# Optimization experiments

Hardware: AMD Instinct MI355X
Metric: run time of the kernel (lower is better)

Reference implementation:

```python
import jax, jax.numpy as jnp
import numpy as np

B, N, DIN, DH = 16, 512, 128, 256
NEG = -9.0e15  # matches -9000000000000000.0 in torch source


def _xavier(key, fan_in, fan_out):
    lim = float(np.sqrt(6.0 / (fan_in + fan_out)))
    return jax.random.uniform(key, (fan_in, fan_out), jnp.float32, -lim, lim)


def _l2n(x, eps=1e-12):
    # torch F.normalize: x / max(||x||, eps)
    return x / jnp.maximum(jnp.linalg.norm(x, axis=-1, keepdims=True), eps)


def _prelu(x, a):
    return jnp.where(x >= 0, x, a * x)


def setup_inputs() -> dict:
    key = jax.random.key(0)
    ks = jax.random.split(key, 12)
    seq = jax.random.normal(ks[0], (B, N, DIN), jnp.float32)
    # sparse-ish nonnegative adjacency with self loops, row-normalized
    u = jax.random.uniform(ks[1], (B, N, N), jnp.float32)
    a = jnp.where(u < 0.1, u, 0.0) + jnp.eye(N, dtype=jnp.float32)[None]
    adj = a / a.sum(-1, keepdims=True)
    # dense diffusion matrix, row-normalized
    d = jax.random.uniform(ks[2], (B, N, N), jnp.float32)
    diff = d / d.sum(-1, keepdims=True)
    # dropout keep-mask for F.dropout(p=0.1, training=True)
    keep = jax.random.bernoulli(ks[3], 0.9, (B, N, N)).astype(jnp.float32)
    drop_mask = keep / 0.9
    return {
        "seq": seq, "adj": adj, "diff": diff, "drop_mask": drop_mask,
        "fc1_w": _xavier(ks[4], DIN, DH),
        "q_w": _xavier(ks[5], DH, DH),
        "k_w": _xavier(ks[6], DH, DH),
        "v_w1": _xavier(ks[7], DH, DH),
        "v_w2": _xavier(ks[8], DH, DH),
        "fc2_w": _xavier(ks[9], DIN, DH),
        "bias1": jnp.zeros((DH,), jnp.float32),
        "bias2": jnp.zeros((DH,), jnp.float32),
        "prelu1_a": jnp.float32(0.25),
        "prelu2_a": jnp.float32(0.25),
        "v_prelu_a": jnp.float32(0.25),
    }


def reference(seq, adj, diff, drop_mask, fc1_w, q_w, k_w, v_w1, v_w2,
              fc2_w, bias1, bias2, prelu1_a, prelu2_a, v_prelu_a):
    # ---- GCN1 (attention branch) ----
    fts = seq @ fc1_w                                   # [B,N,H]
    out = jnp.einsum('bmn,bnh->bmh', adj, fts)          # adj aggregation
    q = _l2n(out @ q_w)
    k = _l2n(out @ k_w)
    scores = jax.lax.stop_gradient(jnp.einsum('bmd,bnd->bmn', q, k))  # .detach()
    div_loss = jnp.mean(jnp.sum((q - k) ** 2, axis=-1))
    att = jnp.where(adj > 0, scores, NEG)
    att = jax.nn.softmax(att, axis=-1) * drop_mask      # dropout(p=0.1)
    agg = jnp.einsum('bmn,bnh->bmh', att, out)
    v = _prelu(agg @ v_w1, v_prelu_a) @ v_w2 + bias1
    h1 = _prelu(v, prelu1_a)
    # ---- GCN2 (plain branch) ----
    h2 = _prelu(jnp.einsum('bmn,bnh->bmh', diff, seq @ fc2_w) + bias2, prelu2_a)
    # ---- Readout ----
    c1 = jnp.mean(h1, axis=1)                           # [B,H]
    c2 = jnp.mean(h2, axis=1)
    # ---- DIS ----
    n1 = _l2n(h1).reshape(B * N, DH)
    n2 = _l2n(h2).reshape(B * N, DH)
    node_logits = n1 @ n2.T                             # [B*N, B*N]
    graph_logits = _l2n(c1) @ _l2n(c2).T                # [B, B]
    return node_logits, graph_logits, div_loss
```

## Files before the change

### kernel.cpp

```cpp
#include <hip/hip_runtime.h>
#include <hip/hip_bf16.h>


using bf16x8 = __attribute__((ext_vector_type(8))) short;
using f32x4  = __attribute__((ext_vector_type(4))) float;

__device__ __forceinline__ unsigned short f2b(float f) {
    union { float f; unsigned int u; } x; x.f = f;
    unsigned int r = x.u + 0x7FFFu + ((x.u >> 16) & 1u);
    return (unsigned short)(r >> 16);
}
__device__ __forceinline__ void gload_lds16(const void* g, void* l) {
    __builtin_amdgcn_global_load_lds(
        (const __attribute__((address_space(1))) void*)g,
        (__attribute__((address_space(3))) void*)l, 16, 0, 0);
}
__device__ __forceinline__ bf16x8 ldfrag(const unsigned short* p) {
    return *reinterpret_cast<const bf16x8*>(p);
}

__global__ __launch_bounds__(256) void prep(
    const float* __restrict__ seq, const float* __restrict__ adj,
    const float* __restrict__ diff,
    const float* __restrict__ fc1, const float* __restrict__ fc2,
    const float* __restrict__ qw,  const float* __restrict__ kw,
    const float* __restrict__ v1,  const float* __restrict__ v2,
    unsigned short* __restrict__ seq_bf, unsigned short* __restrict__ adj_bf,
    unsigned short* __restrict__ diff_bf,
    unsigned short* fc1T, unsigned short* fc2T, unsigned short* qwT,
    unsigned short* kwT,  unsigned short* v1T,  unsigned short* v2T)
{
    __shared__ float t[32][33];
    const int bid = blockIdx.x, tid = threadIdx.x;
    if (bid < 9216) {
        long i = (long)bid * 256 + tid;
        const float* src; unsigned short* dst; long off;
        if (i < 262144)       { src = seq;  dst = seq_bf;  off = i; }
        else if (i < 1310720) { src = adj;  dst = adj_bf;  off = i - 262144; }
        else                  { src = diff; dst = diff_bf; off = i - 1310720; }
        float4 v = reinterpret_cast<const float4*>(src)[off];
        ushort4 o; o.x = f2b(v.x); o.y = f2b(v.y); o.z = f2b(v.z); o.w = f2b(v.w);
        reinterpret_cast<ushort4*>(dst)[off] = o;
        return;
    }
    const int r = bid - 9216;
    const int z = r >> 6;
    const float* in; unsigned short* op; int R;
    if      (z == 0) { in = fc1; op = fc1T; R = 128; }
    else if (z == 1) { in = fc2; op = fc2T; R = 128; }
    else if (z == 2) { in = qw;  op = qwT;  R = 256; }
    else if (z == 3) { in = kw;  op = kwT;  R = 256; }
    else if (z == 4) { in = v1;  op = v1T;  R = 256; }
    else             { in = v2;  op = v2T;  R = 256; }
    const int c0 = (r & 7) * 32, r0 = ((r >> 3) & 7) * 32;
    if (r0 >= R) return;
    const int x = tid & 31, y = tid >> 5;
    for (int i = 0; i < 32; i += 8) t[y + i][x] = in[(long)(r0 + y + i) * 256 + c0 + x];
    __syncthreads();
    for (int i = 0; i < 32; i += 8)
        op[(long)(c0 + y + i) * R + r0 + x] = f2b(t[x][y + i]);
}

#define BN 128
#define BK 64

template<int TBM, bool WF, bool WB, bool SWZ, bool RD>
__global__ __launch_bounds__(256) void gemm_nt(
    const unsigned short* __restrict__ A, const unsigned short* __restrict__ Bt,
    float* __restrict__ Cf, unsigned short* __restrict__ Cb,
    int M, int Nn, int K, int lda, int ldb, int ldc,
    long sA, long sB, long sC,
    const float* __restrict__ rd_psum1, const float* __restrict__ rd_psum2,
    const float* __restrict__ rd_rowpart,
    float* __restrict__ rd_outg, float* __restrict__ rd_outdiv)
{
    constexpr int MI = TBM / 32;
    __shared__ unsigned char smem_g[(TBM + BN) * BK * 2];
    __shared__ float rd_invn[32];
    __shared__ float rd_red[4];
    unsigned short* As = (unsigned short*)smem_g;
    unsigned short* Bs = (unsigned short*)(smem_g + TBM * BK * 2);
    const int b = blockIdx.z;
    A  += (long)b * sA;
    Bt += (long)b * sB;
    const long cbase = (long)b * sC;

    int tx, ty;
    if (SWZ) {
        int bid = blockIdx.y * gridDim.x + blockIdx.x;
        int nwg = gridDim.x * gridDim.y;
        int cpx = nwg >> 3;
        int s = (bid & 7) * cpx + (bid >> 3);
        tx = s % gridDim.x; ty = s / gridDim.x;
    } else { tx = blockIdx.x; ty = blockIdx.y; }
    const int tile_m = ty * TBM;
    const int tile_n = tx * BN;

    const int tid  = threadIdx.x;
    const int lane = tid & 63;
    const int wave = tid >> 6;
    const int wm = (wave >> 1) * (TBM / 2);
    const int wn = (wave & 1) << 6;
    const int lrow = lane >> 3;
    const int lcol = (lane & 7) << 3;

    f32x4 acc[MI][4] = {};

    for (int k0 = 0; k0 < K; k0 += BK) {
        #pragma unroll
        for (int i = 0; i < TBM / 32; ++i) {
            const int rb = (i * 4 + wave) * 8;
            gload_lds16(A + (long)(tile_m + rb + lrow) * lda + k0 + lcol, &As[rb * BK]);
        }
        #pragma unroll
        for (int i = 0; i < 4; ++i) {
            const int rb = (i * 4 + wave) * 8;
            gload_lds16(Bt + (long)(tile_n + rb + lrow) * ldb + k0 + lcol, &Bs[rb * BK]);
        }
        __syncthreads();
        #pragma unroll
        for (int ks = 0; ks < 2; ++ks) {
            const int kk = ks * 32 + ((lane >> 4) << 3);
            bf16x8 af[MI], bq[4];
            #pragma unroll
            for (int mi = 0; mi < MI; ++mi)
                af[mi] = ldfrag(&As[(wm + (lane & 15) + mi * 16) * BK + kk]);
            #pragma unroll
            for (int ni = 0; ni < 4; ++ni)
                bq[ni] = ldfrag(&Bs[(wn + (lane & 15) + ni * 16) * BK + kk]);
            #pragma unroll
            for (int mi = 0; mi < MI; ++mi)
                #pragma unroll
                for (int ni = 0; ni < 4; ++ni)
                    acc[mi][ni] = __builtin_amdgcn_mfma_f32_16x16x32_bf16(
                        af[mi], bq[ni], acc[mi][ni], 0, 0, 0);
        }
        __syncthreads();
    }

    const int c0 = lane & 15;
    const int r0 = (lane >> 4) << 2;

    if (WB) {
        #pragma unroll
        for (int ni = 0; ni < 4; ++ni) {
            const int col = tile_n + wn + ni * 16 + c0;
            #pragma unroll
            for (int mi = 0; mi < MI; ++mi) {
                const int row0 = tile_m + wm + mi * 16 + r0;
                #pragma unroll
                for (int j = 0; j < 4; ++j)
                    Cb[cbase + (long)(row0 + j) * ldc + col] = f2b(acc[mi][ni][j]);
            }
        }
    }
    if (WF) {
        float* bounce = (float*)smem_g;
        const int tr = tid >> 5;
        const int tc = (tid & 31) << 2;
        #pragma unroll
        for (int h = 0; h < 2; ++h) {
            __syncthreads();
            if ((wave >> 1) == h) {
                #pragma unroll
                for (int mi = 0; mi < MI; ++mi)
                    #pragma unroll
                    for (int ni = 0; ni < 4; ++ni)
                        #pragma unroll
                        for (int j = 0; j < 4; ++j)
                            bounce[(mi * 16 + r0 + j) * 128 + wn + ni * 16 + c0] =
                                acc[mi][ni][j];
            }
            __syncthreads();
            #pragma unroll
            for (int p = 0; p < 8; ++p) {
                const int rl = p * 8 + tr;
                f32x4 v = *reinterpret_cast<const f32x4*>(&bounce[rl * 128 + tc]);
                __builtin_nontemporal_store(v, reinterpret_cast<f32x4*>(
                    &Cf[cbase + (long)(tile_m + h * 64 + rl) * ldc + tile_n + tc]));
            }
        }
    }
    if (RD) {
        if (blockIdx.x == 0 && blockIdx.y == 0) {
            __syncthreads();
            float* c1s = (float*)smem_g;
            float* c2s = c1s + 4096;
            const int t = tid;
            for (int g = 0; g < 16; ++g) {
                float s1 = 0.f, s2 = 0.f;
                #pragma unroll
                for (int c = 0; c < 16; ++c) {
                    s1 += rd_psum1[(long)(g * 16 + c) * 256 + t];
                    s2 += rd_psum2[(long)(g * 16 + c) * 256 + t];
                }
                c1s[g * 256 + t] = s1 * (1.f / 512.f);
                c2s[g * 256 + t] = s2 * (1.f / 512.f);
            }
            __syncthreads();
            if (t < 32) {
                const float* row = (t < 16) ? &c1s[t * 256] : &c2s[(t - 16) * 256];
                float ss = 0.f;
                for (int h = 0; h < 256; ++h) { float v = row[h]; ss += v * v; }
                rd_invn[t] = 1.f / fmaxf(sqrtf(ss), 1e-12f);
            }
            __syncthreads();
            const int ii = t >> 4, jj = t & 15;
            float s = 0.f;
            for (int h = 0; h < 256; ++h) s += c1s[ii * 256 + h] * c2s[jj * 256 + h];
            rd_outg[ii * 16 + jj] = s * rd_invn[ii] * rd_invn[16 + jj];
            float ds = 0.f;
            for (int i = t; i < 8192; i += 256) ds += rd_rowpart[i];
            #pragma unroll
            for (int o = 32; o; o >>= 1) ds += __shfl_xor(ds, o);
            if ((t & 63) == 0) rd_red[t >> 6] = ds;
            __syncthreads();
            if (t == 0)
                rd_outdiv[0] = (rd_red[0] + rd_red[1] + rd_red[2] + rd_red[3]) * (1.f / 8192.f);
        }
    }
}

__global__ __launch_bounds__(256) void gcn1qk(
    const unsigned short* __restrict__ adj_bf,
    const unsigned short* __restrict__ ftsT,
    const unsigned short* __restrict__ qkT,
    unsigned short* __restrict__ outT,
    unsigned short* __restrict__ q_bf,
    unsigned short* __restrict__ k_bf)
{
    __shared__ unsigned short Ot[16 * 264];
    __shared__ float sred[16][4];

    const int b  = blockIdx.y;
    const int m0 = blockIdx.x << 4;
    const int tid = threadIdx.x, lane = tid & 63, wave = tid >> 6;
    const int hi = lane >> 4, c0 = lane & 15, r0 = hi << 2;
    const int ko = hi << 3;

    {
        const int wn = wave << 6;
        const unsigned short* ap = adj_bf + ((long)b * 512 + m0 + c0) * 512;
        f32x4 acc[4] = {};
        #pragma unroll 2
        for (int k0 = 0; k0 < 512; k0 += 32) {
            bf16x8 af = ldfrag(ap + k0 + ko);
            #pragma unroll
            for (int ni = 0; ni < 4; ++ni) {
                bf16x8 bq = ldfrag(ftsT + (long)(wn + ni * 16 + c0) * 8192 + b * 512 + k0 + ko);
                acc[ni] = __builtin_amdgcn_mfma_f32_16x16x32_bf16(af, bq, acc[ni], 0, 0, 0);
            }
        }
        #pragma unroll
        for (int ni = 0; ni < 4; ++ni) {
            const int col = wn + ni * 16 + c0;
            ushort4 o;
            unsigned short* e = (unsigned short*)&o;
            #pragma unroll
            for (int j = 0; j < 4; ++j) {
                unsigned short v = f2b(acc[ni][j]);
                e[j] = v;
                Ot[(r0 + j) * 264 + col] = v;
            }
            *reinterpret_cast<ushort4*>(
                &outT[(long)b * 131072 + (long)col * 512 + m0 + r0]) = o;
        }
    }
    __syncthreads();

    {
        const int wn = wave << 7;
        f32x4 acc[8] = {};
        #pragma unroll 2
        for (int k0 = 0; k0 < 256; k0 += 32) {
            bf16x8 af = ldfrag(&Ot[c0 * 264 + k0 + ko]);
            #pragma unroll
            for (int ni = 0; ni < 8; ++ni) {
                bf16x8 bq = ldfrag(qkT + (long)(wn + ni * 16 + c0) * 256 + k0 + ko);
                acc[ni] = __builtin_amdgcn_mfma_f32_16x16x32_bf16(af, bq, acc[ni], 0, 0, 0);
            }
        }
        float rs[4] = {};
        #pragma unroll
        for (int ni = 0; ni < 8; ++ni)
            #pragma unroll
            for (int j = 0; j < 4; ++j) { float x = acc[ni][j]; rs[j] += x * x; }
        #pragma unroll
        for (int o = 1; o <= 8; o <<= 1)
            #pragma unroll
            for (int j = 0; j < 4; ++j) rs[j] += __shfl_xor(rs[j], o);
        if (c0 == 0) {
            #pragma unroll
            for (int j = 0; j < 4; ++j) sred[r0 + j][wave] = rs[j];
        }
        __syncthreads();
        float inv[4];
        #pragma unroll
        for (int j = 0; j < 4; ++j) {
            const int rr = r0 + j;
            float sq = sred[rr][0] + sred[rr][1];
            float sk = sred[rr][2] + sred[rr][3];
            inv[j] = 1.f / fmaxf(sqrtf(wave < 2 ? sq : sk), 1e-12f);
        }
        #pragma unroll
        for (int ni = 0; ni < 8; ++ni)
            #pragma unroll
            for (int j = 0; j < 4; ++j) {
                const long rowg = (long)b * 512 + m0 + r0 + j;
                const int col = wn + ni * 16 + c0;
                unsigned short v = f2b(acc[ni][j] * inv[j]);
                if (wave < 2) q_bf[rowg * 256 + col] = v;
                else          k_bf[rowg * 256 + col - 256] = v;
            }
    }
}

__global__ __launch_bounds__(256) void attmlp_h2(
    const unsigned short* __restrict__ q_bf,
    const unsigned short* __restrict__ k_bf,
    const unsigned short* __restrict__ adj_bf,
    const float* __restrict__ drop,
    const unsigned short* __restrict__ outT,
    const unsigned short* __restrict__ w1T,
    const unsigned short* __restrict__ w2T,
    const float* __restrict__ bias1,
    const float* __restrict__ av, const float* __restrict__ a1,
    unsigned short* __restrict__ n1,
    float* __restrict__ psum1,
    float* __restrict__ rowpart,
    const unsigned short* __restrict__ diff_bf,
    const unsigned short* __restrict__ fts2T,
    const float* __restrict__ bias2, const float* __restrict__ a2,
    unsigned short* __restrict__ n2,
    float* __restrict__ psum2)
{
    __shared__ unsigned char smem[33280];
    __shared__ float redm[32][4], reds[32][4];

    const int idx = blockIdx.x >> 1;
    const int tid = threadIdx.x, lane = tid & 63, wave = tid >> 6;
    const int hi = lane >> 4, c0 = lane & 15, r0 = hi << 2;
    const int ko = hi << 3;

    if (blockIdx.x & 1) {
        unsigned short* Pls = (unsigned short*)smem;
        unsigned short* T   = (unsigned short*)smem;

        const int b  = idx >> 4;
        const int m0 = (idx & 15) << 5;
        const unsigned short* qp = q_bf + (long)b * 131072;
        const unsigned short* kp = k_bf + (long)b * 131072;
        const unsigned short* ot = outT + (long)b * 131072;
        const unsigned short* ap = adj_bf + ((long)b * 512 + m0) * 512;
        const float*          dp = drop   + ((long)b * 512 + m0) * 512;

        {
            const int wn = wave << 7;
            f32x4 acc[2][8] = {};
            #pragma unroll 2
            for (int k0 = 0; k0 < 256; k0 += 32) {
                bf16x8 af[2];
                #pragma unroll
                for (int mi = 0; mi < 2; ++mi)
                    af[mi] = ldfrag(qp + (long)(m0 + mi * 16 + c0) * 256 + k0 + ko);
                #pragma unroll
                for (int ni = 0; ni < 8; ++ni) {
                    bf16x8 bq = ldfrag(kp + (long)(wn + ni * 16 + c0) * 256 + k0 + ko);
                    #pragma unroll
                    for (int mi = 0; mi < 2; ++mi)
                        acc[mi][ni] = __builtin_amdgcn_mfma_f32_16x16x32_bf16(
                            af[mi], bq, acc[mi][ni], 0, 0, 0);
                }
            }

            float rmax[2][4];
            #pragma unroll
            for (int mi = 0; mi < 2; ++mi)
                #pragma unroll
                for (int j = 0; j < 4; ++j) rmax[mi][j] = -3.0e38f;
            #pragma unroll
            for (int mi = 0; mi < 2; ++mi)
                #pragma unroll
                for (int ni = 0; ni < 8; ++ni)
                    #pragma unroll
                    for (int j = 0; j < 4; ++j) {
                        const int rowl = mi * 16 + r0 + j;
                        const int col  = wn + ni * 16 + c0;
                        float s = acc[mi][ni][j];
                        if (col == m0 + rowl)
                            rowpart[(long)b * 512 + m0 + rowl] = 2.f - 2.f * s;
                        bool m = ap[(long)rowl * 512 + col] != 0;
                        s = m ? s : -3.0e38f;
                        acc[mi][ni][j] = s;
                        rmax[mi][j] = fmaxf(rmax[mi][j], s);
                    }
            #pragma unroll
            for (int o = 1; o <= 8; o <<= 1)
                #pragma unroll
                for (int mi = 0; mi < 2; ++mi)
                    #pragma unroll
                    for (int j = 0; j < 4; ++j)
                        rmax[mi][j] = fmaxf(rmax[mi][j], __shfl_xor(rmax[mi][j], o));
            if (c0 == 0) {
                #pragma unroll
                for (int mi = 0; mi < 2; ++mi)
                    #pragma unroll
                    for (int j = 0; j < 4; ++j) redm[mi * 16 + r0 + j][wave] = rmax[mi][j];
            }
            __syncthreads();
            float mx[2][4], rsum[2][4];
            #pragma unroll
            for (int mi = 0; mi < 2; ++mi)
                #pragma unroll
                for (int j = 0; j < 4; ++j) {
                    const int rr = mi * 16 + r0 + j;
                    mx[mi][j] = fmaxf(fmaxf(redm[rr][0], redm[rr][1]),
                                      fmaxf(redm[rr][2], redm[rr][3]));
                    rsum[mi][j] = 0.f;
                }
            #pragma unroll
            for (int mi = 0; mi < 2; ++mi)
                #pragma unroll
                for (int ni = 0; ni < 8; ++ni)
                    #pragma unroll
                    for (int j = 0; j < 4; ++j) {
                        float e = __expf(acc[mi][ni][j] - mx[mi][j]);
                        acc[mi][ni][j] = e;
                        rsum[mi][j] += e;
                    }
            #pragma unroll
            for (int o = 1; o <= 8; o <<= 1)
                #pragma unroll
                for (int mi = 0; mi < 2; ++mi)
                    #pragma unroll
                    for (int j = 0; j < 4; ++j) rsum[mi][j] += __shfl_xor(rsum[mi][j], o);
            if (c0 == 0) {
                #pragma unroll
                for (int mi = 0; mi < 2; ++mi)
                    #pragma unroll
                    for (int j = 0; j < 4; ++j) reds[mi * 16 + r0 + j][wave] = rsum[mi][j];
            }
            __syncthreads();
            float inv[2][4];
            #pragma unroll
            for (int mi = 0; mi < 2; ++mi)
                #pragma unroll
                for (int j = 0; j < 4; ++j) {
                    const int rr = mi * 16 + r0 + j;
                    inv[mi][j] = 1.f / (reds[rr][0] + reds[rr][1] + reds[rr][2] + reds[rr][3]);
                }
            #pragma unroll
            for (int mi = 0; mi < 2; ++mi)
                #pragma unroll
                for (int ni = 0; ni < 8; ++ni)
                    #pragma unroll
                    for (int j = 0; j < 4; ++j) {
                        const int rowl = mi * 16 + r0 + j;
                        const int col  = wn + ni * 16 + c0;
                        float p = acc[mi][ni][j] * inv[mi][j] * dp[(long)rowl * 512 + col];
                        Pls[rowl * 520 + col] = f2b(p);
                    }
        }
        __syncthreads();

        f32x4 acc2[2][4] = {};
        {
            const int wn = wave << 6;
            #pragma unroll 2
            for (int k0 = 0; k0 < 512; k0 += 32) {
                bf16x8 af[2];
                #pragma unroll
                for (int mi = 0; mi < 2; ++mi)
                    af[mi] = ldfrag(&Pls[(mi * 16 + c0) * 520 + k0 + ko]);
                #pragma unroll
                for (int ni = 0; ni < 4; ++ni) {
                    bf16x8 bq = ldfrag(ot + (long)(wn + ni * 16 + c0) * 512 + k0 + ko);
                    #pragma unroll
                    for (int mi = 0; mi < 2; ++mi)
                        acc2[mi][ni] = __builtin_amdgcn_mfma_f32_16x16x32_bf16(
                            af[mi], bq, acc2[mi][ni], 0, 0, 0);
                }
            }
        }
        __syncthreads();

        const int wn6 = wave << 6;
        const float alphav = av[0];
        #pragma unroll
        for (int mi = 0; mi < 2; ++mi)
            #pragma unroll
            for (int ni = 0; ni < 4; ++ni)
                #pragma unroll
                for (int j = 0; j < 4; ++j)
                    T[(mi * 16 + r0 + j) * 264 + wn6 + ni * 16 + c0] = f2b(acc2[mi][ni][j]);
        __syncthreads();
        f32x4 acct[2][4] = {};
        #pragma unroll 2
        for (int k0 = 0; k0 < 256; k0 += 32) {
            bf16x8 af[2];
            #pragma unroll
            for (int mi = 0; mi < 2; ++mi)
                af[mi] = ldfrag(&T[(mi * 16 + c0) * 264 + k0 + ko]);
            #pragma unroll
            for (int ni = 0; ni < 4; ++ni) {
                bf16x8 bq = ldfrag(w1T + (long)(wn6 + ni * 16 + c0) * 256 + k0 + ko);
                #pragma unroll
                for (int mi = 0; mi < 2; ++mi)
                    acct[mi][ni] = __builtin_amdgcn_mfma_f32_16x16x32_bf16(
                        af[mi], bq, acct[mi][ni], 0, 0, 0);
            }
        }
        __syncthreads();
        #pragma unroll
        for (int mi = 0; mi < 2; ++mi)
            #pragma unroll
            for (int ni = 0; ni < 4; ++ni)
                #pragma unroll
                for (int j = 0; j < 4; ++j) {
                    float x = acct[mi][ni][j];
                    x = (x >= 0.f) ? x : alphav * x;
                    T[(mi * 16 + r0 + j) * 264 + wn6 + ni * 16 + c0] = f2b(x);
                }
        __syncthreads();

        f32x4 acc3[2][4] = {};
        #pragma unroll 2
        for (int k0 = 0; k0 < 256; k0 += 32) {
            bf16x8 af[2];
            #pragma unroll
            for (int mi = 0; mi < 2; ++mi)
                af[mi] = ldfrag(&T[(mi * 16 + c0) * 264 + k0 + ko]);
            #pragma unroll
            for (int ni = 0; ni < 4; ++ni) {
                bf16x8 bq = ldfrag(w2T + (long)(wn6 + ni * 16 + c0) * 256 + k0 + ko);
                #pragma unroll
                for (int mi = 0; mi < 2; ++mi)
                    acc3[mi][ni] = __builtin_amdgcn_mfma_f32_16x16x32_bf16(
                        af[mi], bq, acc3[mi][ni], 0, 0, 0);
            }
        }

        const float alpha1 = a1[0];
        float rs[2][4] = {};
        #pragma unroll
        for (int ni = 0; ni < 4; ++ni) {
            const float bv = bias1[wn6 + ni * 16 + c0];
            #pragma unroll
            for (int mi = 0; mi < 2; ++mi)
                #pragma unroll
                for (int j = 0; j < 4; ++j) {
                    float x = acc3[mi][ni][j] + bv;
                    x = (x >= 0.f) ? x : alpha1 * x;
                    acc3[mi][ni][j] = x;
                    rs[mi][j] += x * x;
                }
        }
        #pragma unroll
        for (int o = 1; o <= 8; o <<= 1)
            #pragma unroll
            for (int mi = 0; mi < 2; ++mi)
                #pragma unroll
                for (int j = 0; j < 4; ++j) rs[mi][j] += __shfl_xor(rs[mi][j], o);
        __syncthreads();
        if (c0 == 0) {
            #pragma unroll
            for (int mi = 0; mi < 2; ++mi)
                #pragma unroll
                for (int j = 0; j < 4; ++j) redm[mi * 16 + r0 + j][wave] = rs[mi][j];
        }
        __syncthreads();
        float inv2[2][4];
        #pragma unroll
        for (int mi = 0; mi < 2; ++mi)
            #pragma unroll
            for (int j = 0; j < 4; ++j) {
                const int rr = mi * 16 + r0 + j;
                float s = redm[rr][0] + redm[rr][1] + redm[rr][2] + redm[rr][3];
                inv2[mi][j] = 1.f / fmaxf(sqrtf(s), 1e-12f);
            }
        float cs[4];
        #pragma unroll
        for (int ni = 0; ni < 4; ++ni) {
            float s = 0.f;
            #pragma unroll
            for (int mi = 0; mi < 2; ++mi)
                #pragma unroll
                for (int j = 0; j < 4; ++j) s += acc3[mi][ni][j];
            s += __shfl_xor(s, 16);
            s += __shfl_xor(s, 32);
            cs[ni] = s;
        }
        if (lane < 16) {
            #pragma unroll
            for (int ni = 0; ni < 4; ++ni)
                psum1[(long)idx * 256 + wn6 + ni * 16 + lane] = cs[ni];
        }
        const long row0g = (long)b * 512 + m0;
        #pragma unroll
        for (int mi = 0; mi < 2; ++mi)
            #pragma unroll
            for (int ni = 0; ni < 4; ++ni)
                #pragma unroll
                for (int j = 0; j < 4; ++j)
                    n1[(row0g + mi * 16 + r0 + j) * 256 + wn6 + ni * 16 + c0] =
                        f2b(acc3[mi][ni][j] * inv2[mi][j]);
    } else {
        const int z = idx >> 4;
        const int arow0 = (idx & 15) << 5;
        const unsigned short* ad = diff_bf + (long)z * 262144;
        const unsigned short* bt = fts2T + z * 512;
        const int wn = wave << 6;

        f32x4 acc[2][4] = {};
        #pragma unroll 2
        for (int k0 = 0; k0 < 512; k0 += 32) {
            bf16x8 af[2];
            #pragma unroll
            for (int mi = 0; mi < 2; ++mi)
                af[mi] = ldfrag(ad + (long)(arow0 + mi * 16 + c0) * 512 + k0 + ko);
            #pragma unroll
            for (int ni = 0; ni < 4; ++ni) {
                bf16x8 bq = ldfrag(bt + (long)(wn + ni * 16 + c0) * 8192 + k0 + ko);
                #pragma unroll
                for (int mi = 0; mi < 2; ++mi)
                    acc[mi][ni] = __builtin_amdgcn_mfma_f32_16x16x32_bf16(
                        af[mi], bq, acc[mi][ni], 0, 0, 0);
            }
        }

        const float alpha = a2[0];
        float rs[2][4] = {};
        #pragma unroll
        for (int ni = 0; ni < 4; ++ni) {
            const float bv = bias2[wn + ni * 16 + c0];
            #pragma unroll
            for (int mi = 0; mi < 2; ++mi)
                #pragma unroll
                for (int j = 0; j < 4; ++j) {
                    float x = acc[mi][ni][j] + bv;
                    x = (x >= 0.f) ? x : alpha * x;
                    acc[mi][ni][j] = x;
                    rs[mi][j] += x * x;
                }
        }
        #pragma unroll
        for (int o = 1; o <= 8; o <<= 1)
            #pragma unroll
            for (int mi = 0; mi < 2; ++mi)
                #pragma unroll
                for (int j = 0; j < 4; ++j) rs[mi][j] += __shfl_xor(rs[mi][j], o);
        if (c0 == 0) {
            #pragma unroll
            for (int mi = 0; mi < 2; ++mi)
                #pragma unroll
                for (int j = 0; j < 4; ++j) redm[mi * 16 + r0 + j][wave] = rs[mi][j];
        }
        __syncthreads();
        float inv[2][4];
        #pragma unroll
        for (int mi = 0; mi < 2; ++mi)
            #pragma unroll
            for (int j = 0; j < 4; ++j) {
                const int rr = mi * 16 + r0 + j;
                float s = redm[rr][0] + redm[rr][1] + redm[rr][2] + redm[rr][3];
                inv[mi][j] = 1.f / fmaxf(sqrtf(s), 1e-12f);
            }
        float cs[4];
        #pragma unroll
        for (int ni = 0; ni < 4; ++ni) {
            float s = 0.f;
            #pragma unroll
            for (int mi = 0; mi < 2; ++mi)
                #pragma unroll
                for (int j = 0; j < 4; ++j) s += acc[mi][ni][j];
            s += __shfl_xor(s, 16);
            s += __shfl_xor(s, 32);
            cs[ni] = s;
        }
        if (lane < 16) {
            #pragma unroll
            for (int ni = 0; ni < 4; ++ni)
                psum2[(long)idx * 256 + wn + ni * 16 + lane] = cs[ni];
        }
        const long grow0 = (long)idx * 32;
        #pragma unroll
        for (int mi = 0; mi < 2; ++mi)
            #pragma unroll
            for (int ni = 0; ni < 4; ++ni)
                #pragma unroll
                for (int j = 0; j < 4; ++j)
                    n2[(grow0 + mi * 16 + r0 + j) * 256 + wn + ni * 16 + c0] =
                        f2b(acc[mi][ni][j] * inv[mi][j]);
    }
}

static constexpr long OFF_SEQ_BF  = 0;
static constexpr long OFF_FC1T    = 2097152;
static constexpr long OFF_QWT     = 2228224;
static constexpr long OFF_VW1T    = 2490368;
static constexpr long OFF_VW2T    = 2621440;
static constexpr long OFF_ADJ     = 3145728;
static constexpr long OFF_DIFF    = 11534336;
static constexpr long OFF_FTST    = 19922944;
static constexpr long OFF_OUTT    = 28311552;
static constexpr long OFF_QBF     = 32505856;
static constexpr long OFF_KBF     = 36700160;
static constexpr long OFF_N1      = 40894464;
static constexpr long OFF_N2      = 45088768;
static constexpr long OFF_PSUM    = 49283072;
static constexpr long OFF_ROWPART = 49807360;

extern "C" void kernel_launch(void* const* d_in, const int* in_sizes, int n_in,
                              void* d_out, int out_size, void* d_ws, size_t ws_size,
                              hipStream_t stream) {
    const float* seq      = (const float*)d_in[0];
    const float* adj      = (const float*)d_in[1];
    const float* diff     = (const float*)d_in[2];
    const float* drop     = (const float*)d_in[3];
    const float* fc1_w    = (const float*)d_in[4];
    const float* q_w      = (const float*)d_in[5];
    const float* k_w      = (const float*)d_in[6];
    const float* v_w1     = (const float*)d_in[7];
    const float* v_w2     = (const float*)d_in[8];
    const float* fc2_w    = (const float*)d_in[9];
    const float* bias1    = (const float*)d_in[10];
    const float* bias2    = (const float*)d_in[11];
    const float* prelu1_a = (const float*)d_in[12];
    const float* prelu2_a = (const float*)d_in[13];
    const float* v_prelu  = (const float*)d_in[14];
    float* out = (float*)d_out;

    char* ws = (char*)d_ws;
    unsigned short* seq_bf  = (unsigned short*)(ws + OFF_SEQ_BF);
    unsigned short* fc1T    = (unsigned short*)(ws + OFF_FC1T);
    unsigned short* fc2T    = (unsigned short*)(ws + OFF_FC1T + 65536);
    unsigned short* qwT     = (unsigned short*)(ws + OFF_QWT);
    unsigned short* kwT     = (unsigned short*)(ws + OFF_QWT + 131072);
    unsigned short* vw1T    = (unsigned short*)(ws + OFF_VW1T);
    unsigned short* vw2T    = (unsigned short*)(ws + OFF_VW2T);
    unsigned short* adj_bf  = (unsigned short*)(ws + OFF_ADJ);
    unsigned short* diff_bf = (unsigned short*)(ws + OFF_DIFF);
    unsigned short* ftsT    = (unsigned short*)(ws + OFF_FTST);
    unsigned short* fts2T   = (unsigned short*)(ws + OFF_FTST + 4194304);
    unsigned short* outT    = (unsigned short*)(ws + OFF_OUTT);
    unsigned short* q_bf    = (unsigned short*)(ws + OFF_QBF);
    unsigned short* k_bf    = (unsigned short*)(ws + OFF_KBF);
    unsigned short* n1_bf   = (unsigned short*)(ws + OFF_N1);
    unsigned short* n2_bf   = (unsigned short*)(ws + OFF_N2);
    float*          psum1   = (float*)(ws + OFF_PSUM);
    float*          psum2   = (float*)(ws + OFF_PSUM + 262144);
    float*          rowpart = (float*)(ws + OFF_ROWPART);

    prep<<<9600, 256, 0, stream>>>(seq, adj, diff, fc1_w, fc2_w, q_w, k_w, v_w1, v_w2,
                                   seq_bf, adj_bf, diff_bf, fc1T, fc2T, qwT, kwT, vw1T, vw2T);

    gemm_nt<64, false, true, false, false><<<dim3(64, 4, 2), 256, 0, stream>>>(
        fc1T, seq_bf, nullptr, ftsT,
        256, 8192, 128, 128, 128, 8192, 32768, 0, 2097152,
        nullptr, nullptr, nullptr, nullptr, nullptr);

    gcn1qk<<<dim3(32, 16), 256, 0, stream>>>(adj_bf, ftsT, qwT, outT, q_bf, k_bf);

    attmlp_h2<<<512, 256, 0, stream>>>(
        q_bf, k_bf, adj_bf, drop, outT, vw1T, vw2T, bias1, v_prelu, prelu1_a,
        n1_bf, psum1, rowpart,
        diff_bf, fts2T, bias2, prelu2_a, n2_bf, psum2);

    gemm_nt<128, true, false, true, true><<<dim3(64, 64, 1), 256, 0, stream>>>(
        n1_bf, n2_bf, out, nullptr,
        8192, 8192, 256, 256, 256, 8192, 0, 0, 0,
        psum1, psum2, rowpart, out + 67108864, out + 67109120);

    (void)in_sizes; (void)n_in; (void)out_size; (void)ws_size;
}
```

Before: 195.4 us.

## Enlarge node-logits GEMM to 256x256 tiles with 512 threads

Splits the templated GEMM into a small kernel for the fts projection and a dedicated big kernel for the 8192x8192 node-logit GEMM. The big kernel uses 256x256 output tiles, 8 waves per block, a 1D grid with group swizzling, and a 4-pass LDS bounce for coalesced fp32 stores. The aim is to raise arithmetic intensity and cut global operand reloads on the dominant output-bound GEMM. In exchange it uses 64KB of LDS and 128 accumulator registers per lane, which lowers occupancy.

```diff
diff --git a/kernel.cpp b/kernel.cpp
--- a/kernel.cpp
+++ b/kernel.cpp
@@ -64,72 +64,127 @@
 #define BN 128
 #define BK 64
 
-template<int TBM, bool WF, bool WB, bool SWZ, bool RD>
-__global__ __launch_bounds__(256) void gemm_nt(
+__global__ __launch_bounds__(256) void gemm_small(
     const unsigned short* __restrict__ A, const unsigned short* __restrict__ Bt,
-    float* __restrict__ Cf, unsigned short* __restrict__ Cb,
-    int M, int Nn, int K, int lda, int ldb, int ldc,
-    long sA, long sB, long sC,
+    unsigned short* __restrict__ Cb,
+    int K, int lda, int ldb, int ldc, long sA, long sB, long sC)
+{
+    __shared__ unsigned short As[64 * BK];
+    __shared__ unsigned short Bs[BN * BK];
+    const int b = blockIdx.z;
+    A  += (long)b * sA;
+    Bt += (long)b * sB;
+    const long cbase = (long)b * sC;
+    const int tile_m = blockIdx.y * 64;
+    const int tile_n = blockIdx.x * BN;
+
+    const int tid  = threadIdx.x;
+    const int lane = tid & 63;
+    const int wave = tid >> 6;
+    const int wm = (wave >> 1) * 32;
+    const int wn = (wave & 1) << 6;
+    const int lrow = lane >> 3;
+    const int lcol = (lane & 7) << 3;
+
+    f32x4 acc[2][4] = {};
+
+    for (int k0 = 0; k0 < K; k0 += BK) {
+        #pragma unroll
+        for (int i = 0; i < 2; ++i) {
+            const int rb = (i * 4 + wave) * 8;
+            gload_lds16(A + (long)(tile_m + rb + lrow) * lda + k0 + lcol, &As[rb * BK]);
+        }
+        #pragma unroll
+        for (int i = 0; i < 4; ++i) {
+            const int rb = (i * 4 + wave) * 8;
+            gload_lds16(Bt + (long)(tile_n + rb + lrow) * ldb + k0 + lcol, &Bs[rb * BK]);
+        }
+        __syncthreads();
+        #pragma unroll
+        for (int ks = 0; ks < 2; ++ks) {
+            const int kk = ks * 32 + ((lane >> 4) << 3);
+            bf16x8 af[2], bq[4];
+            #pragma unroll
+            for (int mi = 0; mi < 2; ++mi)
+                af[mi] = ldfrag(&As[(wm + (lane & 15) + mi * 16) * BK + kk]);
+            #pragma unroll
+            for (int ni = 0; ni < 4; ++ni)
+                bq[ni] = ldfrag(&Bs[(wn + (lane & 15) + ni * 16) * BK + kk]);
+            #pragma unroll
+            for (int mi = 0; mi < 2; ++mi)
+                #pragma unroll
+                for (int ni = 0; ni < 4; ++ni)
+                    acc[mi][ni] = __builtin_amdgcn_mfma_f32_16x16x32_bf16(
+                        af[mi], bq[ni], acc[mi][ni], 0, 0, 0);
+        }
+        __syncthreads();
+    }
+
+    const int c0 = lane & 15;
+    const int r0 = (lane >> 4) << 2;
+    #pragma unroll
+    for (int ni = 0; ni < 4; ++ni) {
+        const int col = tile_n + wn + ni * 16 + c0;
+        #pragma unroll
+        for (int mi = 0; mi < 2; ++mi) {
+            const int row0 = tile_m + wm + mi * 16 + r0;
+            #pragma unroll
+            for (int j = 0; j < 4; ++j)
+                Cb[cbase + (long)(row0 + j) * ldc + col] = f2b(acc[mi][ni][j]);
+        }
+    }
+}
+
+__global__ __launch_bounds__(512) void gemm_big(
+    const unsigned short* __restrict__ A,
+    const unsigned short* __restrict__ Bt,
+    float* __restrict__ Cf,
     const float* __restrict__ rd_psum1, const float* __restrict__ rd_psum2,
     const float* __restrict__ rd_rowpart,
     float* __restrict__ rd_outg, float* __restrict__ rd_outdiv)
 {
-    constexpr int MI = TBM / 32;
-    __shared__ unsigned char smem_g[(TBM + BN) * BK * 2];
+    __shared__ unsigned char smem_g[65536];
+    unsigned short* As = (unsigned short*)smem_g;
+    unsigned short* Bs = (unsigned short*)(smem_g + 32768);
     __shared__ float rd_invn[32];
-    __shared__ float rd_red[4];
-    unsigned short* As = (unsigned short*)smem_g;
-    unsigned short* Bs = (unsigned short*)(smem_g + TBM * BK * 2);
-    const int b = blockIdx.z;
-    A  += (long)b * sA;
-    Bt += (long)b * sB;
-    const long cbase = (long)b * sC;
-
-    int tx, ty;
-    if (SWZ) {
-        int bid = blockIdx.y * gridDim.x + blockIdx.x;
-        int nwg = gridDim.x * gridDim.y;
-        int cpx = nwg >> 3;
-        int s = (bid & 7) * cpx + (bid >> 3);
-        tx = s % gridDim.x; ty = s / gridDim.x;
-    } else { tx = blockIdx.x; ty = blockIdx.y; }
-    const int tile_m = ty * TBM;
-    const int tile_n = tx * BN;
+    __shared__ float rd_red[8];
+
+    const int bid = blockIdx.x;
+    const int s = (bid & 7) * 128 + (bid >> 3);
+    const int tx = s & 31, ty = s >> 5;
+    const int tile_m = ty << 8, tile_n = tx << 8;
 
     const int tid  = threadIdx.x;
     const int lane = tid & 63;
     const int wave = tid >> 6;
-    const int wm = (wave >> 1) * (TBM / 2);
-    const int wn = (wave & 1) << 6;
+    const int wr = wave >> 2;
+    const int wc = wave & 3;
     const int lrow = lane >> 3;
     const int lcol = (lane & 7) << 3;
-
-    f32x4 acc[MI][4] = {};
-
-    for (int k0 = 0; k0 < K; k0 += BK) {
-        #pragma unroll
-        for (int i = 0; i < TBM / 32; ++i) {
-            const int rb = (i * 4 + wave) * 8;
-            gload_lds16(A + (long)(tile_m + rb + lrow) * lda + k0 + lcol, &As[rb * BK]);
-        }
+    const int hi = lane >> 4, c0 = lane & 15, r0 = hi << 2;
+
+    f32x4 acc[8][4] = {};
+
+    for (int k0 = 0; k0 < 256; k0 += 64) {
         #pragma unroll
         for (int i = 0; i < 4; ++i) {
-            const int rb = (i * 4 + wave) * 8;
-            gload_lds16(Bt + (long)(tile_n + rb + lrow) * ldb + k0 + lcol, &Bs[rb * BK]);
+            const int rb = (i * 8 + wave) * 8;
+            gload_lds16(A  + (long)(tile_m + rb + lrow) * 256 + k0 + lcol, &As[rb * 64]);
+            gload_lds16(Bt + (long)(tile_n + rb + lrow) * 256 + k0 + lcol, &Bs[rb * 64]);
         }
         __syncthreads();
         #pragma unroll
         for (int ks = 0; ks < 2; ++ks) {
-            const int kk = ks * 32 + ((lane >> 4) << 3);
-            bf16x8 af[MI], bq[4];
-            #pragma unroll
-            for (int mi = 0; mi < MI; ++mi)
-                af[mi] = ldfrag(&As[(wm + (lane & 15) + mi * 16) * BK + kk]);
+            const int kk = ks * 32 + (hi << 3);
+            bf16x8 af[8], bq[4];
+            #pragma unroll
+            for (int mi = 0; mi < 8; ++mi)
+                af[mi] = ldfrag(&As[(wr * 128 + mi * 16 + c0) * 64 + kk]);
             #pragma unroll
             for (int ni = 0; ni < 4; ++ni)
-                bq[ni] = ldfrag(&Bs[(wn + (lane & 15) + ni * 16) * BK + kk]);
-            #pragma unroll
-            for (int mi = 0; mi < MI; ++mi)
+                bq[ni] = ldfrag(&Bs[(wc * 64 + ni * 16 + c0) * 64 + kk]);
+            #pragma unroll
+            for (int mi = 0; mi < 8; ++mi)
                 #pragma unroll
                 for (int ni = 0; ni < 4; ++ni)
                     acc[mi][ni] = __builtin_amdgcn_mfma_f32_16x16x32_bf16(
@@ -138,85 +193,72 @@
         __syncthreads();
     }
 
-    const int c0 = lane & 15;
-    const int r0 = (lane >> 4) << 2;
-
-    if (WB) {
-        #pragma unroll
-        for (int ni = 0; ni < 4; ++ni) {
-            const int col = tile_n + wn + ni * 16 + c0;
-            #pragma unroll
-            for (int mi = 0; mi < MI; ++mi) {
-                const int row0 = tile_m + wm + mi * 16 + r0;
-                #pragma unroll
-                for (int j = 0; j < 4; ++j)
-                    Cb[cbase + (long)(row0 + j) * ldc + col] = f2b(acc[mi][ni][j]);
-            }
+    float* bounce = (float*)smem_g;
+    const int tr8 = tid >> 6;
+    const int tcc = (lane) << 2;
+    #pragma unroll
+    for (int h = 0; h < 4; ++h) {
+        __syncthreads();
+        if (wr == (h >> 1)) {
+            const int mib = (h & 1) * 4;
+            #pragma unroll
+            for (int mm = 0; mm < 4; ++mm)
+                #pragma unroll
+                for (int ni = 0; ni < 4; ++ni)
+                    #pragma unroll
+                    for (int j = 0; j < 4; ++j)
+                        bounce[(mm * 16 + r0 + j) * 256 + wc * 64 + ni * 16 + c0] =
+                            acc[mib + mm][ni][j];
+        }
+        __syncthreads();
+        #pragma unroll
+        for (int p = 0; p < 8; ++p) {
+            const int rl = p * 8 + tr8;
+            f32x4 v = *reinterpret_cast<const f32x4*>(&bounce[rl * 256 + tcc]);
+            __builtin_nontemporal_store(v, reinterpret_cast<f32x4*>(
+                &Cf[(long)(tile_m + h * 64 + rl) * 8192 + tile_n + tcc]));
         }
     }
-    if (WF) {
-        float* bounce = (float*)smem_g;
-        const int tr = tid >> 5;
-        const int tc = (tid & 31) << 2;
-        #pragma unroll
-        for (int h = 0; h < 2; ++h) {
-            __syncthreads();
-            if ((wave >> 1) == h) {
-                #pragma unroll
-                for (int mi = 0; mi < MI; ++mi)
-                    #pragma unroll
-                    for (int ni = 0; ni < 4; ++ni)
-                        #pragma unroll
-                        for (int j = 0; j < 4; ++j)
-                            bounce[(mi * 16 + r0 + j) * 128 + wn + ni * 16 + c0] =
-                                acc[mi][ni][j];
-            }
-            __syncthreads();
-            #pragma unroll
-            for (int p = 0; p < 8; ++p) {
-                const int rl = p * 8 + tr;
-                f32x4 v = *reinterpret_cast<const f32x4*>(&bounce[rl * 128 + tc]);
-                __builtin_nontemporal_store(v, reinterpret_cast<f32x4*>(
-                    &Cf[cbase + (long)(tile_m + h * 64 + rl) * ldc + tile_n + tc]));
-            }
-        }
-    }
-    if (RD) {
-        if (blockIdx.x == 0 && blockIdx.y == 0) {
-            __syncthreads();
-            float* c1s = (float*)smem_g;
-            float* c2s = c1s + 4096;
-            const int t = tid;
-            for (int g = 0; g < 16; ++g) {
-                float s1 = 0.f, s2 = 0.f;
-                #pragma unroll
-                for (int c = 0; c < 16; ++c) {
-                    s1 += rd_psum1[(long)(g * 16 + c) * 256 + t];
-                    s2 += rd_psum2[(long)(g * 16 + c) * 256 + t];
-                }
-                c1s[g * 256 + t] = s1 * (1.f / 512.f);
-                c2s[g * 256 + t] = s2 * (1.f / 512.f);
-            }
-            __syncthreads();
-            if (t < 32) {
-                const float* row = (t < 16) ? &c1s[t * 256] : &c2s[(t - 16) * 256];
-                float ss = 0.f;
-                for (int h = 0; h < 256; ++h) { float v = row[h]; ss += v * v; }
-                rd_invn[t] = 1.f / fmaxf(sqrtf(ss), 1e-12f);
-            }
-            __syncthreads();
-            const int ii = t >> 4, jj = t & 15;
-            float s = 0.f;
-            for (int h = 0; h < 256; ++h) s += c1s[ii * 256 + h] * c2s[jj * 256 + h];
-            rd_outg[ii * 16 + jj] = s * rd_invn[ii] * rd_invn[16 + jj];
-            float ds = 0.f;
-            for (int i = t; i < 8192; i += 256) ds += rd_rowpart[i];
-            #pragma unroll
-            for (int o = 32; o; o >>= 1) ds += __shfl_xor(ds, o);
-            if ((t & 63) == 0) rd_red[t >> 6] = ds;
-            __syncthreads();
-            if (t == 0)
-                rd_outdiv[0] = (rd_red[0] + rd_red[1] + rd_red[2] + rd_red[3]) * (1.f / 8192.f);
+
+    if (bid == 0) {
+        __syncthreads();
+        float* c1s = (float*)smem_g;
+        float* c2s = c1s + 4096;
+        const int t = tid & 255;
+        const int half = tid >> 8;
+        const float* ps = half ? rd_psum2 : rd_psum1;
+        float* cs = half ? c2s : c1s;
+        for (int g = 0; g < 16; ++g) {
+            float s1 = 0.f;
+            #pragma unroll
+            for (int c = 0; c < 16; ++c) s1 += ps[(long)(g * 16 + c) * 256 + t];
+            cs[g * 256 + t] = s1 * (1.f / 512.f);
+        }
+        __syncthreads();
+        if (tid < 32) {
+            const float* row = (tid < 16) ? &c1s[tid * 256] : &c2s[(tid - 16) * 256];
+            float ss = 0.f;
+            for (int hh = 0; hh < 256; ++hh) { float v = row[hh]; ss += v * v; }
+            rd_invn[tid] = 1.f / fmaxf(sqrtf(ss), 1e-12f);
+        }
+        __syncthreads();
+        if (tid < 256) {
+            const int ii = tid >> 4, jj = tid & 15;
+            float s2 = 0.f;
+            for (int hh = 0; hh < 256; ++hh) s2 += c1s[ii * 256 + hh] * c2s[jj * 256 + hh];
+            rd_outg[ii * 16 + jj] = s2 * rd_invn[ii] * rd_invn[16 + jj];
+        }
+        float ds = 0.f;
+        for (int i = tid; i < 8192; i += 512) ds += rd_rowpart[i];
+        #pragma unroll
+        for (int o = 32; o; o >>= 1) ds += __shfl_xor(ds, o);
+        if (lane == 0) rd_red[wave] = ds;
+        __syncthreads();
+        if (tid == 0) {
+            float tot = 0.f;
+            #pragma unroll
+            for (int w = 0; w < 8; ++w) tot += rd_red[w];
+            rd_outdiv[0] = tot * (1.f / 8192.f);
         }
     }
 }
@@ -754,10 +796,8 @@
     prep<<<9600, 256, 0, stream>>>(seq, adj, diff, fc1_w, fc2_w, q_w, k_w, v_w1, v_w2,
                                    seq_bf, adj_bf, diff_bf, fc1T, fc2T, qwT, kwT, vw1T, vw2T);
 
-    gemm_nt<64, false, true, false, false><<<dim3(64, 4, 2), 256, 0, stream>>>(
-        fc1T, seq_bf, nullptr, ftsT,
-        256, 8192, 128, 128, 128, 8192, 32768, 0, 2097152,
-        nullptr, nullptr, nullptr, nullptr, nullptr);
+    gemm_small<<<dim3(64, 4, 2), 256, 0, stream>>>(
+        fc1T, seq_bf, ftsT, 128, 128, 128, 8192, 32768, 0, 2097152);
 
     gcn1qk<<<dim3(32, 16), 256, 0, stream>>>(adj_bf, ftsT, qwT, outT, q_bf, k_bf);
 
@@ -766,9 +806,8 @@
         n1_bf, psum1, rowpart,
         diff_bf, fts2T, bias2, prelu2_a, n2_bf, psum2);
 
-    gemm_nt<128, true, false, true, true><<<dim3(64, 64, 1), 256, 0, stream>>>(
-        n1_bf, n2_bf, out, nullptr,
-        8192, 8192, 256, 256, 256, 8192, 0, 0, 0,
+    gemm_big<<<1024, 512, 0, stream>>>(
+        n1_bf, n2_bf, out,
         psum1, psum2, rowpart, out + 67108864, out + 67109120);
 
     (void)in_sizes; (void)n_in; (void)out_size; (void)ws_size;
```

After: 200.4 us. +2.6%, slower.
